# Optimization experiments

Hardware: AMD Instinct MI355X
Metric: run time of the kernel (lower is better)

## Reference

```python
import math
import numpy as np
import jax
import jax.numpy as jnp

B_IN, B_L1, B_L2 = 10, 6, 3
BATCH, NUM_POINTS = 4, 512
F1, F2, F_OUT = 8, 16, 10
NB = BATCH * NUM_POINTS
N_GRID_S2, N_GRID_SO3 = 24, 144


def _lf(n):
    return math.lgamma(n + 1)


def wigner_d(l, beta):
    """Wigner small-d matrices d^l_{m',m}(beta). beta: np [K] -> [K, 2l+1, 2l+1]."""
    beta = np.asarray(beta, dtype=np.float64)
    K = beta.shape[0]
    d = np.zeros((K, 2 * l + 1, 2 * l + 1))
    c, s = np.cos(beta / 2.0), np.sin(beta / 2.0)
    for mi, mp in enumerate(range(-l, l + 1)):
        for ni, m in enumerate(range(-l, l + 1)):
            k0, k1 = max(0, m - mp), min(l + m, l - mp)
            acc = np.zeros(K)
            for k in range(k0, k1 + 1):
                lg = 0.5 * (_lf(l + mp) + _lf(l - mp) + _lf(l + m) + _lf(l - m)) - _lf(l + m - k) - _lf(k) - _lf(mp - m + k) - _lf(l - mp - k)
                acc = acc + ((-1.0) ** (mp - m + k)) * np.exp(lg) * c ** (2 * l - 2 * k + m - mp) * s ** (mp - m + 2 * k)
            d[:, mi, ni] = acc
    return d


def quad_beta_weights(b):
    """Driscoll-Healy quadrature betas and weights at bandwidth b."""
    k = np.arange(2 * b)
    beta = np.pi * (2 * k + 1) / (4 * b)
    j = np.arange(b)[:, None]
    w = (2.0 / b) * np.sin(beta) * np.sum(np.sin((2 * j + 1) * beta[None, :]) / (2 * j + 1), axis=0)
    return beta, w


# near-identity kernel grids (as in s2cnn): s2 grid 3 betas x 8 alphas, so3 grid x 6 gammas
_b = np.arange(1, 4) * (np.pi / 8) / 3
_a = np.linspace(0, 2 * np.pi, 8, endpoint=False)
_GB1, _GA1 = [g.ravel() for g in np.meshgrid(_b, _a, indexing='ij')]
_g = np.linspace(0, 2 * np.pi, 6, endpoint=False)
_GB2, _GA2, _GG2 = [g.ravel() for g in np.meshgrid(_b, _a, _g, indexing='ij')]

_BETA_IN, _W_IN = quad_beta_weights(B_IN)
_BETA_L1, _W_L1 = quad_beta_weights(B_L1)
_BETA_L2, _W_L2 = quad_beta_weights(B_L2)

# S2 FFT tables: quadrature-weighted d^l_{m,0}(beta_k), l < b_l1
_S2FFT_D = [jnp.asarray((wigner_d(l, _BETA_IN)[:, :, l] * _W_IN[:, None]).astype(np.complex64)) for l in range(B_L1)]
# S2 kernel basis psi1[l]: [24, 2l+1] = d^l_{m,0}(beta_g) e^{-i m alpha_g}
_PSI1 = []
for l in range(B_L1):
    m = np.arange(-l, l + 1)
    _PSI1.append(jnp.asarray((wigner_d(l, _GB1)[:, :, l] * np.exp(-1j * m[None, :] * _GA1[:, None])).astype(np.complex64)))
# SO3 inverse-FFT d matrices at b_l1 quadrature betas
_D_L1 = [jnp.asarray(wigner_d(l, _BETA_L1).astype(np.complex64)) for l in range(B_L1)]
# SO3 FFT tables at b_l1 (output bandwidth b_l2)
_SO3FFT_D = [jnp.asarray((wigner_d(l, _BETA_L1) * _W_L1[:, None, None]).astype(np.complex64)) for l in range(B_L2)]
# SO3 kernel basis psi2[l]: [144, 2l+1, 2l+1] = e^{-i m a} d^l_{mn}(b) e^{-i n g}
_PSI2 = []
for l in range(B_L2):
    m = np.arange(-l, l + 1)
    ph = np.exp(-1j * m[None, :, None] * _GA2[:, None, None]) * np.exp(-1j * m[None, None, :] * _GG2[:, None, None])
    _PSI2.append(jnp.asarray((wigner_d(l, _GB2) * ph).astype(np.complex64)))
_D_L2 = [jnp.asarray(wigner_d(l, _BETA_L2).astype(np.complex64)) for l in range(B_L2)]
_W_INT = jnp.asarray(_W_L2.astype(np.float32))


def s2_fft(x, b_out):
    # x: [n, f, 2b(beta), 2b(alpha)] real -> list_l of [n, f, 2l+1] complex
    two_b = x.shape[-1]
    F = jnp.fft.fft(x, axis=-1)
    out = []
    for l in range(b_out):
        idx = np.arange(-l, l + 1) % two_b
        out.append(jnp.einsum('nfkm,km->nfm', F[..., idx], _S2FFT_D[l]))
    return out


def so3_ifft_list(z, b_out, d_list):
    # z[l]: [n, fo, 2l+1(m), 2l+1(p)] -> real [n, fo, 2b(beta), 2b(alpha), 2b(gamma)]
    n2 = 2 * b_out
    n, fo = z[0].shape[:2]
    Fh = jnp.zeros((n, fo, n2, n2, n2), jnp.complex64)
    for l in range(b_out):
        idx = np.arange(-l, l + 1) % n2
        blk = (2 * l + 1) * jnp.einsum('nomp,kmp->nokmp', z[l], d_list[l])
        Fh = Fh.at[:, :, :, idx[:, None], idx[None, :]].add(blk)
    return jnp.real(jnp.fft.ifft2(Fh, axes=(-2, -1)) * (n2 * n2))


def s2_conv(x, w, bias):
    xs = s2_fft(x, B_L1)
    wc = w.astype(jnp.complex64)
    z = []
    for l in range(B_L1):
        y = jnp.einsum('iog,gm->iom', wc, _PSI1[l])  # kernel spectrum [fi, fo, 2l+1]
        z.append(jnp.einsum('nim,iop->nomp', xs[l], jnp.conj(y)))
    return so3_ifft_list(z, B_L1, _D_L1) + bias[None, :, None, None, None]


def so3_fft(x, b_out):
    # x: [n, f, 2b(beta), 2b(alpha), 2b(gamma)] -> list_l of [n, f, 2l+1, 2l+1]
    two_b = x.shape[-1]
    F = jnp.fft.fft2(x, axes=(-2, -1))
    out = []
    for l in range(b_out):
        idx = np.arange(-l, l + 1) % two_b
        out.append(jnp.einsum('nfkmp,kmp->nfmp', F[:, :, :, idx[:, None], idx[None, :]], _SO3FFT_D[l]))
    return out


def so3_conv(x, w, bias):
    xs = so3_fft(x, B_L2)
    wc = w.astype(jnp.complex64)
    z = []
    for l in range(B_L2):
        y = jnp.einsum('iog,gmp->iomp', wc, _PSI2[l])  # [fi, fo, 2l+1, 2l+1]
        z.append(jnp.einsum('nimk,iopk->nomp', xs[l], jnp.conj(y)))
    return so3_ifft_list(z, B_L2, _D_L2) + bias[None, :, None, None, None]


def so3_integrate(x):
    # mean over alpha, gamma; quadrature-weighted sum over beta
    return jnp.einsum('nfk,k->nf', x.mean(axis=(-2, -1)), _W_INT)


def forward(x, w1, b1, w2, b2, w_out, bias_out):
    h = jax.nn.relu(s2_conv(x, w1, b1))
    h = jax.nn.relu(so3_conv(h, w2, b2))
    feat = so3_integrate(h).reshape(BATCH, NUM_POINTS, F2).transpose(0, 2, 1)  # [B, F2, P]
    pooled = feat.max(axis=-1)  # MaxPool1d(kernel_size=num_points) + squeeze
    return pooled @ w_out.T + bias_out


def setup_inputs():
    ks = jax.random.split(jax.random.key(0), 4)
    return {
        'x': jax.random.normal(ks[0], (NB, 1, 2 * B_IN, 2 * B_IN), jnp.float32),
        'w1': jax.random.normal(ks[1], (1, F1, N_GRID_S2), jnp.float32) * 0.1,
        'b1': jnp.zeros((F1,), jnp.float32),
        'w2': jax.random.normal(ks[2], (F1, F2, N_GRID_SO3), jnp.float32) * 0.05,
        'b2': jnp.zeros((F2,), jnp.float32),
        'w_out': jax.random.normal(ks[3], (F_OUT, F2), jnp.float32) * 0.1,
        'bias_out': jnp.zeros((F_OUT,), jnp.float32),
    }


def reference(x, w1, b1, w2, b2, w_out, bias_out):
    return forward(x, w1, b1, w2, b2, w_out, bias_out)
```

## Files before the change

kernel.cpp:

```cpp
#include <hip/hip_runtime.h>
#include <cmath>

typedef float2 c32;

__device__ __forceinline__ void cmadd(c32& acc, c32 a, float cr, float ci){
    acc.x += a.x*cr - a.y*ci;
    acc.y += a.x*ci + a.y*cr;
}

__host__ __device__ constexpr int M12(int x){ return ((x%12)+12)%12; }
__host__ __device__ constexpr int M6(int x){ return ((x%6)+6)%6; }

#define SQ32 0.86602540378443864676f
#define RT22 0.70710678118654752440f
static constexpr float CW12[12] = {1.f, SQ32, 0.5f, 0.f, -0.5f, -SQ32, -1.f, -SQ32, -0.5f, 0.f, 0.5f, SQ32};
static constexpr float SW12[12] = {0.f, 0.5f, SQ32, 1.f, SQ32, 0.5f, 0.f, -0.5f, -SQ32, -1.f, -SQ32, -0.5f};
static constexpr float CW6[6] = {1.f, 0.5f, -0.5f, -1.f, -0.5f, 0.5f};
static constexpr float SW6[6] = {0.f, SQ32, SQ32, 0.f, -SQ32, -SQ32};
static constexpr float CW8[8] = {1.f, RT22, 0.f, -RT22, -1.f, -RT22, 0.f, RT22};
static constexpr float SW8[8] = {0.f, RT22, 1.f, RT22, 0.f, -RT22, -1.f, -RT22};
static constexpr float CW20_[6] = {1.f, 0.95105651629515357212f, 0.80901699437494742410f,
                                   0.58778525229247312917f, 0.30901699437494742410f, 0.f};
static constexpr float SW20_[6] = {0.f, 0.30901699437494742410f, 0.58778525229247312917f,
                                   0.80901699437494742410f, 0.95105651629515357212f, 1.f};

#define O_CY1  0
#define O_CY2P 528
#define O_XS   (O_CY2P + 14080)
#define O_XS2P (O_XS + 73728)
#define N_C32_TOTAL (O_XS2P + 2048*8*30)

#define O_S2D  0
#define O_D1SG 1320
#define O_D2SG 1518
#define O_WINT 1743
#define O_D1S  1752
#define O_DG   (O_D1S + 6336)
#define O_D2P  (O_DG + 360)
#define O_FEAT (O_D2P + 360)

#define DPI 3.14159265358979323846

__device__ __forceinline__ void cell_decode(int c, int& L, int& m, int& p){
    int base;
    if (c < 1){ L=0; base=0; } else if (c < 6){ L=1; base=1; }
    else if (c < 15){ L=2; base=6; } else if (c < 28){ L=3; base=15; }
    else if (c < 45){ L=4; base=28; } else { L=5; base=45; }
    int r = c - base;
    if (r < 2*L){ m = r>>1; p = (r&1)? L : -L; }
    else { m = L; p = (r - 2*L) - L; }
}

static constexpr double FCT[13] = {1.,1.,2.,6.,24.,120.,720.,5040.,40320.,
                                   362880.,3628800.,39916800.,479001600.};

__device__ __forceinline__ double dipow(double b, int e){
    double r = 1.0;
    while (e){ if (e & 1) r *= b; b *= b; e >>= 1; }
    return r;
}

__device__ double dev_wig(int l, int mp, int m, double beta){
    int k0 = max(0, m - mp), k1 = min(l + m, l - mp);
    double c = cos(0.5*beta), s = sin(0.5*beta);
    double fnum = sqrt(FCT[l+mp]*FCT[l-mp]*FCT[l+m]*FCT[l-m]);
    double acc = 0.0;
    for (int k = k0; k <= k1; ++k){
        double t = fnum / (FCT[l+m-k]*FCT[k]*FCT[mp-m+k]*FCT[l-mp-k])
                 * dipow(c, 2*l-2*k+m-mp) * dipow(s, mp-m+2*k);
        acc += ((mp-m+k) & 1) ? -t : t;
    }
    return acc;
}

__device__ double dev_qw(int b, double beta){
    double s = 0.0;
    for (int j = 0; j < b; ++j) s += sin((2.0*j+1.0)*beta)/(2.0*j+1.0);
    return (2.0/b)*sin(beta)*s;
}

__global__ __launch_bounds__(256) void k_setup_pre(float* fb){
    int gid = blockIdx.x*256 + threadIdx.x;
    if (gid < 198){
        int pi = gid%11; int t = gid/11; int ib = t%3; int l = t/3;
        float v = 0.f;
        if (pi < 2*l+1){ double beta = (ib+1)*DPI/24.0; v = (float)dev_wig(l, pi-l, 0, beta); }
        fb[O_D1SG+gid] = v; return;
    }
    gid -= 198;
    if (gid < 225){
        int qi = gid%5; int t = gid/5; int pi = t%5; t /= 5; int ib = t%3; int l = t/3;
        float v = 0.f;
        if (pi < 2*l+1 && qi < 2*l+1){ double beta = (ib+1)*DPI/24.0; v = (float)dev_wig(l, pi-l, qi-l, beta); }
        fb[O_D2SG+gid] = v; return;
    }
    gid -= 225;
    if (gid < 6){ double beta = DPI*(2*gid+1)/12.0; fb[O_WINT+gid] = (float)dev_qw(3, beta); return; }
}

__global__ __launch_bounds__(256) void k_setup_main(c32* cb, float* fb,
                                                    const float* __restrict__ w1,
                                                    const float* __restrict__ w2){
    __shared__ float wsh[144];
    __shared__ c32 W1s[3][8][5];
    __shared__ c32 Rs[3][5][5];
    int bid = blockIdx.x, tid = threadIdx.x;
    if (bid < 128){
        int o = bid >> 3, i = bid & 7;
        for (int c = tid; c < 144; c += 256) wsh[c] = w2[(i*16+o)*144 + c];
        __syncthreads();
        for (int c = tid; c < 120; c += 256){
            int ib = c/40, r = c%40, ia = r/5, qi = r%5;
            int q = qi - 2; int qm = ((q%6)+6)%6;
            float wr = CW6[qm], wi = SW6[qm];
            float er = 1.f, ei = 0.f, sx = 0.f, sy = 0.f;
            const float* wrow = wsh + ib*48 + ia*6;
            #pragma unroll
            for (int ig = 0; ig < 6; ++ig){
                float w = wrow[ig];
                sx += w*er; sy += w*ei;
                float nr = er*wr - ei*wi; ei = er*wi + ei*wr; er = nr;
            }
            W1s[ib][ia][qi] = make_float2(sx, sy);
        }
        __syncthreads();
        for (int c = tid; c < 75; c += 256){
            int ib = c/25, r = c%25, pi = r/5, qi = r%5;
            int p = pi - 2; int pm = ((p%8)+8)%8;
            float wr = CW8[pm], wi = SW8[pm];
            float er = 1.f, ei = 0.f;
            c32 acc = make_float2(0.f,0.f);
            #pragma unroll
            for (int ia = 0; ia < 8; ++ia){
                c32 wv = W1s[ib][ia][qi];
                acc.x += wv.x*er - wv.y*ei;
                acc.y += wv.x*ei + wv.y*er;
                float nr = er*wr - ei*wi; ei = er*wi + ei*wr; er = nr;
            }
            Rs[ib][pi][qi] = acc;
        }
        __syncthreads();
        for (int c = tid; c < 110; c += 256){
            int cell = c/5, qt = c%5;
            int l, p;
            if (cell == 0){ l=0; p=0; }
            else if (cell < 7){ l=1; p=(cell-1)%3 - 1; }
            else { l=2; p=(cell-7)%5 - 2; }
            c32 acc = make_float2(0.f,0.f);
            if (qt < 2*l+1){
                int q = qt - l;
                #pragma unroll
                for (int ib = 0; ib < 3; ++ib){
                    float d = fb[O_D2SG + (l*3+ib)*25 + (p+l)*5 + (q+l)];
                    c32 rv = Rs[ib][p+2][q+2];
                    acc.x += d*rv.x; acc.y += d*rv.y;
                }
            }
            cb[O_CY2P + ((o*22+cell)*8 + i)*5 + qt] = acc;
        }
        return;
    }
    int gid = (bid-128)*256 + tid;
    if (gid < 1320){
        int mi = gid%11; int t = gid/11; int k = t%20; int l = t/20;
        float v = 0.f;
        if (mi < 2*l+1){
            double beta = DPI*(2*k+1)/40.0;
            v = (float)(dev_wig(l, mi-l, 0, beta) * dev_qw(10, beta));
        }
        fb[O_S2D+gid] = v; return;
    }
    gid -= 1320;
    if (gid < 528){
        int pi = gid%11; int t = gid/11; int l = t%6; int o = t/6;
        c32 acc = make_float2(0.f,0.f);
        if (pi < 2*l+1){
            int p = pi - l;
            int pm = ((p%8)+8)%8;
            float wr = CW8[pm], wi = SW8[pm];
            for (int ib = 0; ib < 3; ++ib){
                float d = fb[O_D1SG + (l*3+ib)*11 + pi];
                float er = 1.f, ei = 0.f, sx = 0.f, sy = 0.f;
                #pragma unroll
                for (int ia = 0; ia < 8; ++ia){
                    float w = w1[o*24 + ib*8 + ia];
                    sx += w*er; sy += w*ei;
                    float nr = er*wr - ei*wi; ei = er*wi + ei*wr; er = nr;
                }
                acc.x += d*sx; acc.y += d*sy;
            }
        }
        cb[O_CY1 + (o*6+l)*11 + pi] = acc;
        return;
    }
    gid -= 528;
    if (gid < 6336){
        int k = gid%12; int t = gid/12; int l = t%8; int cell = t/8;
        int L, m, p; cell_decode(cell, L, m, p);
        float v = 0.f;
        if (l < 6 && l >= L){
            double beta = DPI*(2*k+1)/24.0;
            v = (float)dev_wig(l, m, p, beta);
        }
        fb[O_D1S+gid] = v; return;
    }
    gid -= 6336;
    if (gid < 360){
        int k = gid%12; int slot = gid/12;
        int lm = slot/5, qt = slot%5;
        int l = lm==0?0:(lm<3?1:2);
        int m = lm==0?0:(lm<3?lm-1:lm-3);
        float v = 0.f;
        if (qt < 2*l+1){
            double beta = DPI*(2*k+1)/24.0;
            v = (float)(dev_wig(l, m, qt-l, beta) * dev_qw(6, beta));
        }
        fb[O_DG+gid] = v; return;
    }
    gid -= 360;
    if (gid < 360){
        int lp = gid%4; int t = gid/4; int k = t%6; int cell = t/6;
        int m = cell/5, pi = cell%5, p = pi-2, ap = p<0?-p:p;
        float v = 0.f;
        if (lp < 3 && lp >= m && lp >= ap){
            double beta = DPI*(2*k+1)/12.0;
            v = (float)dev_wig(lp, m, p, beta);
        }
        fb[O_D2P+gid] = v; return;
    }
}

__global__ __launch_bounds__(64) void k_s2fft(const float* __restrict__ x, const float* __restrict__ fb,
                                              c32* __restrict__ XS){
    __shared__ float xsh[400];
    __shared__ c32 F1[20][6];
    int n = blockIdx.x, tid = threadIdx.x;
    for (int i = tid; i < 400; i += 64) xsh[i] = x[n*400 + i];
    __syncthreads();
    for (int i = tid; i < 120; i += 64){
        int k = i/6, m = i%6;
        float wr = CW20_[m], wi = -SW20_[m];
        float er = 1.f, ei = 0.f, ax = 0.f, ay = 0.f;
        const float* row = xsh + k*20;
        #pragma unroll
        for (int a = 0; a < 20; ++a){
            float v = row[a];
            ax += v*er; ay += v*ei;
            float nr = er*wr - ei*wi; ei = er*wi + ei*wr; er = nr;
        }
        F1[k][m] = make_float2(ax, ay);
    }
    __syncthreads();
    if (tid < 36){
        int l = 0; while ((l+1)*(l+1) <= tid) ++l;
        int mi = tid - l*l; int m = mi - l;
        c32 acc = make_float2(0.f,0.f);
        for (int k = 0; k < 20; ++k){
            float d = fb[O_S2D + (l*20+k)*11 + mi];
            c32 F = (m >= 0) ? F1[k][m] : make_float2(F1[k][-m].x, -F1[k][-m].y);
            acc.x += d*F.x; acc.y += d*F.y;
        }
        XS[n*36 + tid] = acc;
    }
}

__global__ __launch_bounds__(256) void k_layer1(const c32* __restrict__ cb, const float* __restrict__ fb,
                                                const float* __restrict__ b1, c32* __restrict__ xs2p){
    __shared__ c32 xs_sh[36];
    __shared__ c32 u1[864];
    __shared__ c32 u2[936];
    __shared__ c32 Gg[432];
    __shared__ c32 Gs[180];
    int tid = threadIdx.x;
    int n = blockIdx.x >> 3, o = blockIdx.x & 7;
    float bias = b1[o];
    if (tid < 36) xs_sh[tid] = cb[O_XS + n*36 + tid];
    __syncthreads();

    for (int c = tid; c < 396; c += 256){
        int l = c/66, mp = c - l*66, m = mp/11, pi = mp - m*11;
        int p = pi - 5, ap = p < 0 ? -p : p;
        c32 v = make_float2(0.f, 0.f);
        if (m <= l && ap <= l){
            c32 a = xs_sh[l*l + l + m];
            c32 b = cb[O_CY1 + o*66 + l*11 + p + l];
            float f = (float)(2*l+1);
            v.x = f*(a.x*b.x - a.y*b.y); v.y = f*(a.x*b.y + a.y*b.x);
        }
        u1[c] = v;
    }
    __syncthreads();

    if (tid < 132){
        int cell = tid >> 1, kh = tid & 1;
        int L, m, p; cell_decode(cell, L, m, p);
        int mp = m*11 + p + 5;
        c32 acc[6];
        #pragma unroll
        for (int j = 0; j < 6; ++j) acc[j] = make_float2(0.f,0.f);
        for (int l = L; l < 6; ++l){
            c32 z = u1[l*66 + mp];
            const float* dp = fb + O_D1S + (cell*8 + l)*12 + kh*6;
            #pragma unroll
            for (int j = 0; j < 6; ++j){
                float d = dp[j];
                acc[j].x += d*z.x; acc[j].y += d*z.y;
            }
        }
        #pragma unroll
        for (int j = 0; j < 6; ++j) u2[mp*12 + kh*6 + j] = acc[j];
    }
    __syncthreads();

    if (tid < 72){
        int m = tid/12, k = tid - m*12;
        c32 S0 = u2[(m*11+5)*12 + k];
        c32 E[5], O[5];
        #pragma unroll
        for (int p = 1; p <= 5; ++p){
            c32 a = u2[(m*11+5+p)*12 + k], b = u2[(m*11+5-p)*12 + k];
            E[p-1] = make_float2(a.x+b.x, a.y+b.y);
            O[p-1] = make_float2(a.x-b.x, a.y-b.y);
        }
        #pragma unroll
        for (int g = 0; g < 6; ++g){
            float vex=0.f, vey=0.f, vox=0.f, voy=0.f;
            #pragma unroll
            for (int p = 1; p <= 5; ++p){
                const float cc = CW12[M12(p*g)], ss = SW12[M12(p*g)];
                float vx = E[p-1].x*cc - O[p-1].y*ss;
                float vy = E[p-1].y*cc + O[p-1].x*ss;
                if (p & 1){ vox += vx; voy += vy; } else { vex += vx; vey += vy; }
            }
            float tex = S0.x + vex, tey = S0.y + vey;
            u1[(m*12+g)*12 + k]   = make_float2(tex + vox, tey + voy);
            u1[(m*12+g+6)*12 + k] = make_float2(tex - vox, tey - voy);
        }
    }
    __syncthreads();

    float* hh = (float*)u2;
    if (tid < 144){
        int g = tid/12, k = tid - g*12;
        c32 t1 = u1[(1*12+g)*12+k], t2 = u1[(2*12+g)*12+k], t3 = u1[(3*12+g)*12+k];
        c32 t4 = u1[(4*12+g)*12+k], t5 = u1[(5*12+g)*12+k];
        float base = u1[(0*12+g)*12+k].x + bias;
        #pragma unroll
        for (int a = 0; a < 6; ++a){
            float od = t1.x*CW12[M12(1*a)] - t1.y*SW12[M12(1*a)]
                     + t3.x*CW12[M12(3*a)] - t3.y*SW12[M12(3*a)]
                     + t5.x*CW12[M12(5*a)] - t5.y*SW12[M12(5*a)];
            float ev = t2.x*CW12[M12(2*a)] - t2.y*SW12[M12(2*a)]
                     + t4.x*CW12[M12(4*a)] - t4.y*SW12[M12(4*a)];
            float h0 = base + 2.f*(ev+od);
            float h1 = base + 2.f*(ev-od);
            hh[(g*12+a)*13+k]     = h0 > 0.f ? h0 : 0.f;
            hh[(g*12+a+6)*13+k]   = h1 > 0.f ? h1 : 0.f;
        }
    }
    __syncthreads();

    if (tid < 144){
        int a = tid/12, k = tid - a*12;
        float hv[12];
        #pragma unroll
        for (int g = 0; g < 12; ++g) hv[g] = hh[(g*12+a)*13+k];
        float s0 = 0.f;
        #pragma unroll
        for (int g = 0; g < 12; ++g) s0 += hv[g];
        Gg[a*12+k] = make_float2(s0, 0.f);
        #pragma unroll
        for (int mg = 1; mg < 3; ++mg){
            float ax = 0.f, ay = 0.f;
            #pragma unroll
            for (int g = 0; g < 12; ++g){
                const int tt = M12(mg*g);
                ax += hv[g]*CW12[tt]; ay -= hv[g]*SW12[tt];
            }
            Gg[(mg*12+a)*12+k] = make_float2(ax, ay);
        }
    }
    __syncthreads();

    if (tid < 108){
        int j = tid/36, r = tid - j*36, mg = r/12, k = r - mg*12;
        const c32* gp = Gg + mg*144 + k;
        if (j == 0){
            float sx = 0.f, sy = 0.f;
            #pragma unroll
            for (int a = 0; a < 6; ++a){
                c32 xa = gp[a*12], ya = gp[(a+6)*12];
                sx += xa.x + ya.x; sy += xa.y + ya.y;
            }
            Gs[(2*3+mg)*12+k] = make_float2(sx, sy);
        } else if (j == 1){
            float Cx=0.f,Cy=0.f,Sx=0.f,Sy=0.f;
            #pragma unroll
            for (int a = 0; a < 6; ++a){
                c32 xa = gp[a*12], ya = gp[(a+6)*12];
                float ux = xa.x - ya.x, uy = xa.y - ya.y;
                const float cc = CW12[a], ss = SW12[a];
                Cx += ux*cc; Cy += uy*cc;
                Sx += ux*ss; Sy += uy*ss;
            }
            Gs[(3*3+mg)*12+k] = make_float2(Cx + Sy, Cy - Sx);
            Gs[(1*3+mg)*12+k] = make_float2(Cx - Sy, Cy + Sx);
        } else {
            float Cx=0.f,Cy=0.f,Sx=0.f,Sy=0.f;
            #pragma unroll
            for (int a = 0; a < 6; ++a){
                c32 xa = gp[a*12], ya = gp[(a+6)*12];
                float ux = xa.x + ya.x, uy = xa.y + ya.y;
                const float cc = CW12[M12(2*a)], ss = SW12[M12(2*a)];
                Cx += ux*cc; Cy += uy*cc;
                Sx += ux*ss; Sy += uy*ss;
            }
            Gs[(4*3+mg)*12+k] = make_float2(Cx + Sy, Cy - Sx);
            Gs[(0*3+mg)*12+k] = make_float2(Cx - Sy, Cy + Sx);
        }
    }
    __syncthreads();

    if (tid < 30){
        int lm = tid/5, qt = tid - lm*5;
        int l = lm==0?0:(lm<3?1:2);
        int m = lm==0?0:(lm<3?lm-1:lm-3);
        c32 acc = make_float2(0.f,0.f);
        if (qt < 2*l+1){
            int q = qt - l;
            #pragma unroll
            for (int k = 0; k < 12; ++k){
                float d = fb[O_DG + tid*12 + k];
                c32 gvv;
                if (q >= 0) gvv = Gs[((m+2)*3 + q)*12 + k];
                else { c32 w = Gs[((2-m)*3 + (-q))*12 + k]; gvv = make_float2(w.x, -w.y); }
                acc.x += d*gvv.x; acc.y += d*gvv.y;
            }
        }
        xs2p[(n*8+o)*30 + tid] = acc;
    }
}

__global__ __launch_bounds__(256) void k_layer2(const c32* __restrict__ cb, const float* __restrict__ fb,
                                                const float* __restrict__ b2, float* __restrict__ feat){
    __shared__ c32 xs2sh[960];
    __shared__ c32 zp2[4][384];
    __shared__ c32 T2[1728];
    __shared__ float part[576];
    int tid = threadIdx.x, n0 = blockIdx.x*4;
    for (int c = tid; c < 960; c += 256) xs2sh[c] = cb[O_XS2P + n0*240 + c];
    __syncthreads();

    for (int c = tid; c < 1408; c += 256){
        int nl = c/352, cc = c - nl*352, o = cc/22, cell = cc - o*22;
        int l, lm;
        if (cell == 0){ l=0; lm=0; }
        else if (cell < 7){ l=1; lm=1+(cell-1)/3; }
        else { l=2; lm=3+(cell-7)/5; }
        const c32* cy = cb + O_CY2P + (o*22+cell)*40;
        const c32* xv0 = xs2sh + nl*240;
        c32 acc = make_float2(0.f,0.f);
        #pragma unroll
        for (int i = 0; i < 8; ++i){
            #pragma unroll
            for (int qt = 0; qt < 5; ++qt){
                c32 xv = xv0[(i*6+lm)*5 + qt];
                c32 yv = cy[i*5+qt];
                acc.x += xv.x*yv.x - xv.y*yv.y;
                acc.y += xv.x*yv.y + xv.y*yv.x;
            }
        }
        float f = (float)(2*l+1);
        zp2[nl][o*24+cell] = make_float2(f*acc.x, f*acc.y);
    }
    __syncthreads();

    for (int nl = 0; nl < 4; ++nl){
        for (int c = tid; c < 288; c += 256){
            int o = c/18, r = c - o*18, k = r/3, m = r - k*3;
            c32 s2v[5];
            #pragma unroll
            for (int pi = 0; pi < 5; ++pi){
                const int p = pi-2; const int ap = p<0?-p:p;
                c32 acc = make_float2(0.f,0.f);
                #pragma unroll
                for (int l = 0; l < 3; ++l){
                    if (l >= ap){
                        float d = fb[O_D2P + ((m*5+pi)*6+k)*4 + l];
                        int cell = (l==0) ? 0 : ((l==1) ? 1+m*3+(p+1) : 7+m*5+(p+2));
                        c32 z = zp2[nl][o*24+cell];
                        acc.x += d*z.x; acc.y += d*z.y;
                    }
                }
                s2v[pi] = acc;
            }
            #pragma unroll
            for (int g = 0; g < 6; ++g){
                c32 t = make_float2(0.f,0.f);
                #pragma unroll
                for (int pi = 0; pi < 5; ++pi){
                    const int tt = M6((pi-2)*g);
                    cmadd(t, s2v[pi], CW6[tt], SW6[tt]);
                }
                T2[((o*6+k)*3+m)*6+g] = t;
            }
        }
        __syncthreads();
        for (int c = tid; c < 576; c += 256){
            int o = c/36, r = c - o*36, k = r/6, g = r - k*6;
            c32 t0 = T2[((o*6+k)*3+0)*6+g];
            c32 t1 = T2[((o*6+k)*3+1)*6+g];
            c32 t2 = T2[((o*6+k)*3+2)*6+g];
            float base = t0.x + b2[o];
            float s = 0.f;
            #pragma unroll
            for (int a = 0; a < 6; ++a){
                float h = base + 2.f*(t1.x*CW6[M6(a)]   - t1.y*SW6[M6(a)])
                               + 2.f*(t2.x*CW6[M6(2*a)] - t2.y*SW6[M6(2*a)]);
                s += h > 0.f ? h : 0.f;
            }
            part[c] = s * fb[O_WINT + k];
        }
        __syncthreads();
        if (tid < 16){
            float s = 0.f;
            #pragma unroll
            for (int j = 0; j < 36; ++j) s += part[tid*36+j];
            feat[(n0+nl)*16+tid] = s * (1.f/36.f);
        }
        __syncthreads();
    }
}

__global__ __launch_bounds__(256) void k_poolhead(const float* __restrict__ feat,
                                                  const float* __restrict__ w_out,
                                                  const float* __restrict__ bias_out,
                                                  float* __restrict__ out){
    __shared__ float red[256];
    __shared__ float pool_s[64];
    int tid = threadIdx.x;
    int pair = tid >> 2, chunk = tid & 3;
    int b = pair >> 4, o = pair & 15;
    float m = -3.4e38f;
    for (int j = 0; j < 128; ++j){
        int pt = chunk*128 + j;
        m = fmaxf(m, feat[(b*512+pt)*16 + o]);
    }
    red[tid] = m;
    __syncthreads();
    if (tid < 64){
        pool_s[tid] = fmaxf(fmaxf(red[tid*4], red[tid*4+1]),
                            fmaxf(red[tid*4+2], red[tid*4+3]));
    }
    __syncthreads();
    if (tid < 40){
        int bb = tid/10, jj = tid%10;
        float s = bias_out[jj];
        #pragma unroll
        for (int oo = 0; oo < 16; ++oo) s += pool_s[bb*16+oo]*w_out[jj*16+oo];
        out[tid] = s;
    }
}

extern "C" void kernel_launch(void* const* d_in, const int* in_sizes, int n_in,
                              void* d_out, int out_size, void* d_ws, size_t ws_size,
                              hipStream_t stream){
    const float* x        = (const float*)d_in[0];
    const float* w1       = (const float*)d_in[1];
    const float* b1       = (const float*)d_in[2];
    const float* w2       = (const float*)d_in[3];
    const float* b2       = (const float*)d_in[4];
    const float* w_out    = (const float*)d_in[5];
    const float* bias_out = (const float*)d_in[6];
    float* out = (float*)d_out;

    c32*   cb = (c32*)d_ws;
    float* fb = (float*)(cb + N_C32_TOTAL);
    float* feat = fb + O_FEAT;

    k_setup_pre<<<2, 256, 0, stream>>>(fb);
    k_setup_main<<<163, 256, 0, stream>>>(cb, fb, w1, w2);
    k_s2fft<<<2048, 64, 0, stream>>>(x, fb, cb + O_XS);
    k_layer1<<<2048*8, 256, 0, stream>>>(cb, fb, b1, cb + O_XS2P);
    k_layer2<<<512, 256, 0, stream>>>(cb, fb, b2, feat);
    k_poolhead<<<1, 256, 0, stream>>>(feat, w_out, bias_out, out);
}
```

Baseline: 198.7 us.

## Pack two output channels per layer1 block, batch s2fft, split pooling

```diff
diff --git a/kernel.cpp b/kernel.cpp
--- a/kernel.cpp
+++ b/kernel.cpp
@@ -38,6 +38,7 @@
 #define O_DG   (O_D1S + 6336)
 #define O_D2P  (O_DG + 360)
 #define O_FEAT (O_D2P + 360)
+#define O_POOL (O_FEAT + 32768)
 
 #define DPI 3.14159265358979323846
 
@@ -230,54 +231,55 @@
     }
 }
 
-__global__ __launch_bounds__(64) void k_s2fft(const float* __restrict__ x, const float* __restrict__ fb,
-                                              c32* __restrict__ XS){
-    __shared__ float xsh[400];
-    __shared__ c32 F1[20][6];
-    int n = blockIdx.x, tid = threadIdx.x;
-    for (int i = tid; i < 400; i += 64) xsh[i] = x[n*400 + i];
-    __syncthreads();
-    for (int i = tid; i < 120; i += 64){
-        int k = i/6, m = i%6;
+__global__ __launch_bounds__(256) void k_s2fft(const float* __restrict__ x, const float* __restrict__ fb,
+                                               c32* __restrict__ XS){
+    __shared__ float xsh[1600];
+    __shared__ c32 F1[4][20][6];
+    int n0 = blockIdx.x*4, tid = threadIdx.x;
+    for (int i = tid; i < 1600; i += 256) xsh[i] = x[n0*400 + i];
+    __syncthreads();
+    for (int i = tid; i < 480; i += 256){
+        int nl = i/120, r = i - nl*120, k = r/6, m = r - k*6;
         float wr = CW20_[m], wi = -SW20_[m];
         float er = 1.f, ei = 0.f, ax = 0.f, ay = 0.f;
-        const float* row = xsh + k*20;
+        const float* row = xsh + nl*400 + k*20;
         #pragma unroll
         for (int a = 0; a < 20; ++a){
             float v = row[a];
             ax += v*er; ay += v*ei;
             float nr = er*wr - ei*wi; ei = er*wi + ei*wr; er = nr;
         }
-        F1[k][m] = make_float2(ax, ay);
-    }
-    __syncthreads();
-    if (tid < 36){
-        int l = 0; while ((l+1)*(l+1) <= tid) ++l;
-        int mi = tid - l*l; int m = mi - l;
+        F1[nl][k][m] = make_float2(ax, ay);
+    }
+    __syncthreads();
+    if (tid < 144){
+        int nl = tid/36, t = tid - nl*36;
+        int l = 0; while ((l+1)*(l+1) <= t) ++l;
+        int mi = t - l*l; int m = mi - l;
         c32 acc = make_float2(0.f,0.f);
         for (int k = 0; k < 20; ++k){
             float d = fb[O_S2D + (l*20+k)*11 + mi];
-            c32 F = (m >= 0) ? F1[k][m] : make_float2(F1[k][-m].x, -F1[k][-m].y);
+            c32 F = (m >= 0) ? F1[nl][k][m] : make_float2(F1[nl][k][-m].x, -F1[nl][k][-m].y);
             acc.x += d*F.x; acc.y += d*F.y;
         }
-        XS[n*36 + tid] = acc;
+        XS[(n0+nl)*36 + t] = acc;
     }
 }
 
 __global__ __launch_bounds__(256) void k_layer1(const c32* __restrict__ cb, const float* __restrict__ fb,
                                                 const float* __restrict__ b1, c32* __restrict__ xs2p){
     __shared__ c32 xs_sh[36];
-    __shared__ c32 u1[864];
-    __shared__ c32 u2[936];
-    __shared__ c32 Gg[432];
-    __shared__ c32 Gs[180];
+    __shared__ c32 u1[2][864];
+    __shared__ c32 u2[2][936];
     int tid = threadIdx.x;
-    int n = blockIdx.x >> 3, o = blockIdx.x & 7;
+    int half = tid >> 7, r = tid & 127;
+    int n = blockIdx.x >> 2, oh = blockIdx.x & 3;
+    int o = oh*2 + half;
     float bias = b1[o];
     if (tid < 36) xs_sh[tid] = cb[O_XS + n*36 + tid];
     __syncthreads();
 
-    for (int c = tid; c < 396; c += 256){
+    for (int c = r; c < 396; c += 128){
         int l = c/66, mp = c - l*66, m = mp/11, pi = mp - m*11;
         int p = pi - 5, ap = p < 0 ? -p : p;
         c32 v = make_float2(0.f, 0.f);
@@ -287,38 +289,38 @@
             float f = (float)(2*l+1);
             v.x = f*(a.x*b.x - a.y*b.y); v.y = f*(a.x*b.y + a.y*b.x);
         }
-        u1[c] = v;
-    }
-    __syncthreads();
-
-    if (tid < 132){
-        int cell = tid >> 1, kh = tid & 1;
+        u1[half][c] = v;
+    }
+    __syncthreads();
+
+    if (r < 66){
+        int cell = r;
         int L, m, p; cell_decode(cell, L, m, p);
         int mp = m*11 + p + 5;
-        c32 acc[6];
-        #pragma unroll
-        for (int j = 0; j < 6; ++j) acc[j] = make_float2(0.f,0.f);
+        c32 acc[12];
+        #pragma unroll
+        for (int j = 0; j < 12; ++j) acc[j] = make_float2(0.f,0.f);
         for (int l = L; l < 6; ++l){
-            c32 z = u1[l*66 + mp];
-            const float* dp = fb + O_D1S + (cell*8 + l)*12 + kh*6;
-            #pragma unroll
-            for (int j = 0; j < 6; ++j){
+            c32 z = u1[half][l*66 + mp];
+            const float* dp = fb + O_D1S + (cell*8 + l)*12;
+            #pragma unroll
+            for (int j = 0; j < 12; ++j){
                 float d = dp[j];
                 acc[j].x += d*z.x; acc[j].y += d*z.y;
             }
         }
         #pragma unroll
-        for (int j = 0; j < 6; ++j) u2[mp*12 + kh*6 + j] = acc[j];
-    }
-    __syncthreads();
-
-    if (tid < 72){
-        int m = tid/12, k = tid - m*12;
-        c32 S0 = u2[(m*11+5)*12 + k];
+        for (int j = 0; j < 12; ++j) u2[half][mp*12 + j] = acc[j];
+    }
+    __syncthreads();
+
+    if (r < 72){
+        int m = r/12, k = r - m*12;
+        c32 S0 = u2[half][(m*11+5)*12 + k];
         c32 E[5], O[5];
         #pragma unroll
         for (int p = 1; p <= 5; ++p){
-            c32 a = u2[(m*11+5+p)*12 + k], b = u2[(m*11+5-p)*12 + k];
+            c32 a = u2[half][(m*11+5+p)*12 + k], b = u2[half][(m*11+5-p)*12 + k];
             E[p-1] = make_float2(a.x+b.x, a.y+b.y);
             O[p-1] = make_float2(a.x-b.x, a.y-b.y);
         }
@@ -333,18 +335,18 @@
                 if (p & 1){ vox += vx; voy += vy; } else { vex += vx; vey += vy; }
             }
             float tex = S0.x + vex, tey = S0.y + vey;
-            u1[(m*12+g)*12 + k]   = make_float2(tex + vox, tey + voy);
-            u1[(m*12+g+6)*12 + k] = make_float2(tex - vox, tey - voy);
-        }
-    }
-    __syncthreads();
-
-    float* hh = (float*)u2;
-    if (tid < 144){
-        int g = tid/12, k = tid - g*12;
-        c32 t1 = u1[(1*12+g)*12+k], t2 = u1[(2*12+g)*12+k], t3 = u1[(3*12+g)*12+k];
-        c32 t4 = u1[(4*12+g)*12+k], t5 = u1[(5*12+g)*12+k];
-        float base = u1[(0*12+g)*12+k].x + bias;
+            u1[half][(m*12+g)*12 + k]   = make_float2(tex + vox, tey + voy);
+            u1[half][(m*12+g+6)*12 + k] = make_float2(tex - vox, tey - voy);
+        }
+    }
+    __syncthreads();
+
+    float* hh = (float*)u2[half];
+    for (int c = r; c < 144; c += 128){
+        int g = c/12, k = c - g*12;
+        c32 t1 = u1[half][(1*12+g)*12+k], t2 = u1[half][(2*12+g)*12+k], t3 = u1[half][(3*12+g)*12+k];
+        c32 t4 = u1[half][(4*12+g)*12+k], t5 = u1[half][(5*12+g)*12+k];
+        float base = u1[half][(0*12+g)*12+k].x + bias;
         #pragma unroll
         for (int a = 0; a < 6; ++a){
             float od = t1.x*CW12[M12(1*a)] - t1.y*SW12[M12(1*a)]
@@ -360,8 +362,10 @@
     }
     __syncthreads();
 
-    if (tid < 144){
-        int a = tid/12, k = tid - a*12;
+    c32* Gg = u1[half];
+    c32* Gs = u1[half] + 432;
+    for (int c = r; c < 144; c += 128){
+        int a = c/12, k = c - a*12;
         float hv[12];
         #pragma unroll
         for (int g = 0; g < 12; ++g) hv[g] = hh[(g*12+a)*13+k];
@@ -382,8 +386,8 @@
     }
     __syncthreads();
 
-    if (tid < 108){
-        int j = tid/36, r = tid - j*36, mg = r/12, k = r - mg*12;
+    if (r < 108){
+        int j = r/36, rr = r - j*36, mg = rr/12, k = rr - mg*12;
         const c32* gp = Gg + mg*144 + k;
         if (j == 0){
             float sx = 0.f, sy = 0.f;
@@ -421,8 +425,8 @@
     }
     __syncthreads();
 
-    if (tid < 30){
-        int lm = tid/5, qt = tid - lm*5;
+    if (r < 30){
+        int lm = r/5, qt = r - lm*5;
         int l = lm==0?0:(lm<3?1:2);
         int m = lm==0?0:(lm<3?lm-1:lm-3);
         c32 acc = make_float2(0.f,0.f);
@@ -430,14 +434,14 @@
             int q = qt - l;
             #pragma unroll
             for (int k = 0; k < 12; ++k){
-                float d = fb[O_DG + tid*12 + k];
+                float d = fb[O_DG + r*12 + k];
                 c32 gvv;
                 if (q >= 0) gvv = Gs[((m+2)*3 + q)*12 + k];
                 else { c32 w = Gs[((2-m)*3 + (-q))*12 + k]; gvv = make_float2(w.x, -w.y); }
                 acc.x += d*gvv.x; acc.y += d*gvv.y;
             }
         }
-        xs2p[(n*8+o)*30 + tid] = acc;
+        xs2p[(n*8+o)*30 + r] = acc;
     }
 }
 
@@ -532,32 +536,23 @@
     }
 }
 
-__global__ __launch_bounds__(256) void k_poolhead(const float* __restrict__ feat,
-                                                  const float* __restrict__ w_out,
-                                                  const float* __restrict__ bias_out,
-                                                  float* __restrict__ out){
-    __shared__ float red[256];
-    __shared__ float pool_s[64];
+__global__ __launch_bounds__(64) void k_pool(const float* __restrict__ feat, float* __restrict__ pool){
+    int b = blockIdx.x >> 4, o = blockIdx.x & 15;
     int tid = threadIdx.x;
-    int pair = tid >> 2, chunk = tid & 3;
-    int b = pair >> 4, o = pair & 15;
     float m = -3.4e38f;
-    for (int j = 0; j < 128; ++j){
-        int pt = chunk*128 + j;
+    for (int pt = tid; pt < 512; pt += 64)
         m = fmaxf(m, feat[(b*512+pt)*16 + o]);
-    }
-    red[tid] = m;
-    __syncthreads();
-    if (tid < 64){
-        pool_s[tid] = fmaxf(fmaxf(red[tid*4], red[tid*4+1]),
-                            fmaxf(red[tid*4+2], red[tid*4+3]));
-    }
-    __syncthreads();
+    for (int off = 32; off; off >>= 1) m = fmaxf(m, __shfl_down(m, off));
+    if (tid == 0) pool[b*16 + o] = m;
+}
+
+__global__ __launch_bounds__(64) void k_head(const float* __restrict__ pool, const float* __restrict__ w_out,
+                                             const float* __restrict__ bias_out, float* __restrict__ out){
+    int tid = threadIdx.x;
     if (tid < 40){
-        int bb = tid/10, jj = tid%10;
-        float s = bias_out[jj];
-        #pragma unroll
-        for (int oo = 0; oo < 16; ++oo) s += pool_s[bb*16+oo]*w_out[jj*16+oo];
+        int b = tid/10, j = tid%10;
+        float s = bias_out[j];
+        for (int o = 0; o < 16; ++o) s += pool[b*16+o]*w_out[j*16+o];
         out[tid] = s;
     }
 }
@@ -577,11 +572,13 @@
     c32*   cb = (c32*)d_ws;
     float* fb = (float*)(cb + N_C32_TOTAL);
     float* feat = fb + O_FEAT;
+    float* pool = fb + O_POOL;
 
     k_setup_pre<<<2, 256, 0, stream>>>(fb);
     k_setup_main<<<163, 256, 0, stream>>>(cb, fb, w1, w2);
-    k_s2fft<<<2048, 64, 0, stream>>>(x, fb, cb + O_XS);
-    k_layer1<<<2048*8, 256, 0, stream>>>(cb, fb, b1, cb + O_XS2P);
+    k_s2fft<<<512, 256, 0, stream>>>(x, fb, cb + O_XS);
+    k_layer1<<<2048*4, 256, 0, stream>>>(cb, fb, b1, cb + O_XS2P);
     k_layer2<<<512, 256, 0, stream>>>(cb, fb, b2, feat);
-    k_poolhead<<<1, 256, 0, stream>>>(feat, w_out, bias_out, out);
-}
+    k_pool<<<64, 64, 0, stream>>>(feat, pool);
+    k_head<<<1, 64, 0, stream>>>(pool, w_out, bias_out, out);
+}
```

Result: faster. 180.2 us (-9.4%).
